# Kernel optimization log

Hardware: AMD Instinct MI355X
Metric: run time of the kernel (lower is better)

The kernel has to match this reference:

```python
import jax, jax.numpy as jnp
import numpy as np

# EventPropLinear constants (match init_kwargs)
DT = 1.0
TAU_M = 10.0
TAU_S = 1.0
AM = 1.0 - DT / TAU_M   # membrane decay
BM = DT / TAU_M         # membrane input coupling
AS = 1.0 - DT / TAU_S   # synaptic decay


def setup_inputs() -> dict:
    key = jax.random.key(0)
    k1, k2 = jax.random.split(key)
    T, B, IN, OUT = 128, 64, 1024, 1024
    x = jax.random.uniform(k1, (T, B, IN), dtype=jnp.float32)  # input drive / spikes in [0,1)
    # torch.nn.init.normal_(weight, mu, mu) with mu=0.1 -> mean 0.1, std 0.1
    weight = 0.1 + 0.1 * jax.random.normal(k2, (OUT, IN), dtype=jnp.float32)
    return {"x": x, "weight": weight}


def _forward_core(x, weight):
    # x: [T, B, IN]; weight: [OUT, IN]
    T, B, _ = x.shape
    O = weight.shape[0]
    # step i (1..T-1) uses input[i-1]; precompute the linear drive once
    cur = jnp.einsum('tbi,oi->tbo', x[:-1], weight)  # [T-1, B, OUT]

    def step(carry, c):
        V, I = carry
        Vn = AM * V + BM * I
        In = AS * I + c
        s = (Vn > 1.0).astype(x.dtype)
        Vn = (1.0 - s) * Vn           # reset on spike
        return (Vn, In), (s, In)

    z = jnp.zeros((B, O), x.dtype)
    _, (spk, Iseq) = jax.lax.scan(step, (z, z), cur)
    zrow = jnp.zeros((1, B, O), x.dtype)
    out = jnp.concatenate([zrow, spk], axis=0)      # output[0] = 0
    I_full = jnp.concatenate([zrow, Iseq], axis=0)  # I[0] = 0
    return out, I_full


def reference(x, weight):
    # returns spike train [T, B, OUT], matching torch output permuted back to time-major
    return _forward_core(x, weight)[0]
```

## Files before the change

kernel.cpp:

```cpp
#include <hip/hip_runtime.h>
#include <hip/hip_fp8.h>

typedef __attribute__((ext_vector_type(8))) short short8;
typedef __attribute__((ext_vector_type(4))) float f32x4;

__device__ __forceinline__ unsigned short f2bf(float f) {
    unsigned u = __float_as_uint(f);
    u += 0x7FFFu + ((u >> 16) & 1u);
    return (unsigned short)(u >> 16);
}

__device__ __forceinline__ unsigned char f2fp8(float f) {
    __hip_fp8_e4m3 q(f);
    return q.__x;
}

__global__ void eventprop_cvt8_kernel(const float* __restrict__ x, const float* __restrict__ w,
                                      unsigned char* __restrict__ x8, unsigned char* __restrict__ w8,
                                      const int nx, const int ntot)
{
    const int i = blockIdx.x * blockDim.x + threadIdx.x;
    const int e0 = i * 8;
    if (e0 >= ntot) return;
    const float* src;
    unsigned char* dst;
    if (e0 < nx) { src = x + e0; dst = x8 + e0; }
    else         { src = w + (e0 - nx); dst = w8 + (e0 - nx); }
    const float4 f0 = *(const float4*)(src);
    const float4 f1 = *(const float4*)(src + 4);
    uchar4 a, b;
    a.x = f2fp8(f0.x); a.y = f2fp8(f0.y); a.z = f2fp8(f0.z); a.w = f2fp8(f0.w);
    b.x = f2fp8(f1.x); b.y = f2fp8(f1.y); b.z = f2fp8(f1.z); b.w = f2fp8(f1.w);
    uint2 v;
    v.x = *(unsigned int*)&a;
    v.y = *(unsigned int*)&b;
    *(uint2*)dst = v;
}

__global__ __launch_bounds__(256, 4) void eventprop_gemm_scan_fp8_kernel(
    const unsigned char* __restrict__ X8, const unsigned char* __restrict__ W8,
    float* __restrict__ out, const int K, const int N, const int nbn)
{
    __shared__ __align__(16) unsigned char smem[33280];
    unsigned char* As = smem;
    unsigned char* Bs = smem + 16384;
    unsigned short* cur16 = (unsigned short*)smem;

    const int bid0 = blockIdx.x;
    const int cpx = gridDim.x >> 3;
    const int bid = (bid0 & 7) * cpx + (bid0 >> 3);
    const int bm = bid / nbn, bn = bid % nbn;
    const int n0 = bn * 128;

    const int tid = threadIdx.x;
    const int lane = tid & 63;
    const int wave = tid >> 6;
    const int wr = wave >> 1, wc = wave & 1;
    const int lrow = lane & 15, kg = lane >> 4;
    const int srow = lane >> 3;
    const int scol = (((lane & 7) ^ srow) * 16);

    f32x4 acc[4][4] = {};

    for (int kt = 0; kt < K; kt += 128) {
        #pragma unroll
        for (int jj = 0; jj < 4; ++jj) {
            const int j = wave * 4 + jj;
            const int trow = j * 8 + srow;
            const unsigned char* ga = &X8[(size_t)(trow * 64 + bm) * K + kt + scol];
            __builtin_amdgcn_global_load_lds(
                (const __attribute__((address_space(1))) unsigned int*)ga,
                (__attribute__((address_space(3))) unsigned int*)&As[j * 1024], 16, 0, 0);
        }
        #pragma unroll
        for (int jj = 0; jj < 4; ++jj) {
            const int j = wave * 4 + jj;
            const int row = j * 8 + srow;
            const unsigned char* gb = &W8[(size_t)(n0 + row) * K + kt + scol];
            __builtin_amdgcn_global_load_lds(
                (const __attribute__((address_space(1))) unsigned int*)gb,
                (__attribute__((address_space(3))) unsigned int*)&Bs[j * 1024], 16, 0, 0);
        }
        __syncthreads();

        const int rx = (lrow & 7) << 4;
        #pragma unroll
        for (int ks = 0; ks < 4; ++ks) {
            const int cc = (ks * 32 + kg * 8) ^ rx;
            long a[4], b[4];
            #pragma unroll
            for (int mi = 0; mi < 4; ++mi)
                a[mi] = *(const long*)&As[(wr * 64 + mi * 16 + lrow) * 128 + cc];
            #pragma unroll
            for (int ni = 0; ni < 4; ++ni)
                b[ni] = *(const long*)&Bs[(wc * 64 + ni * 16 + lrow) * 128 + cc];
            #pragma unroll
            for (int mi = 0; mi < 4; ++mi)
                #pragma unroll
                for (int ni = 0; ni < 4; ++ni)
                    acc[mi][ni] = __builtin_amdgcn_mfma_f32_16x16x32_fp8_fp8(
                        a[mi], b[ni], acc[mi][ni], 0, 0, 0);
        }
        __syncthreads();
    }

    const int r0 = kg * 4;
    #pragma unroll
    for (int mi = 0; mi < 4; ++mi) {
        #pragma unroll
        for (int ni = 0; ni < 4; ++ni) {
            #pragma unroll
            for (int r = 0; r < 4; ++r) {
                const int t = wr * 64 + mi * 16 + r0 + r;
                const int col = wc * 64 + ni * 16 + lrow;
                cur16[t * 130 + col] = f2bf(acc[mi][ni][r]);
            }
        }
    }
    __syncthreads();

    if (tid < 128) {
        const int col = tid;
        const size_t obase = (size_t)bm * N + n0 + col;
        const int BO = 64 * N;
        float V = 0.f, I = 0.f;
        float c[8];
        #pragma unroll
        for (int p = 0; p < 8; ++p)
            c[p] = __uint_as_float((unsigned int)cur16[p * 130 + col] << 16);
        out[obase] = 0.f;
        #pragma unroll 1
        for (int i = 0; i < 120; i += 8) {
            #pragma unroll
            for (int p = 0; p < 8; ++p) {
                const int it = i + p;
                const float cn = __uint_as_float((unsigned int)cur16[(it + 8) * 130 + col] << 16);
                const float Vn = 0.9f * V + 0.1f * I;
                const float s = (Vn > 1.0f) ? 1.0f : 0.0f;
                I = c[p];
                V = (1.0f - s) * Vn;
                out[(size_t)(it + 1) * BO + obase] = s;
                c[p] = cn;
            }
        }
        #pragma unroll
        for (int p = 0; p < 7; ++p) {
            const int it = 120 + p;
            const float Vn = 0.9f * V + 0.1f * I;
            const float s = (Vn > 1.0f) ? 1.0f : 0.0f;
            I = c[p];
            V = (1.0f - s) * Vn;
            out[(size_t)(it + 1) * BO + obase] = s;
        }
    }
}

__global__ __launch_bounds__(256, 2) void eventprop_gemm_f32in_kernel(
    const float* __restrict__ X, const float* __restrict__ W, float* __restrict__ C,
    const int K, const int N, const int nbn)
{
    __shared__ unsigned short As[128][32];
    __shared__ unsigned short Bs[128][32];
    const int bid = blockIdx.x;
    const int bm = bid / nbn, bn = bid % nbn;
    const int m0 = bm * 128, n0 = bn * 128;
    const int tid = threadIdx.x;
    const int lane = tid & 63;
    const int wave = tid >> 6;
    const int wr = wave >> 1, wc = wave & 1;
    const int lrow = lane & 15, kg = lane >> 4;

    f32x4 acc[4][4] = {};
    for (int kt = 0; kt < K; kt += 32) {
        #pragma unroll
        for (int p = 0; p < 4; ++p) {
            const int idx = p * 256 + tid;
            const int row = idx >> 3;
            const int c4  = (idx & 7) * 4;
            const float4 fa = *(const float4*)&X[(size_t)(m0 + row) * K + kt + c4];
            ushort4 ua; ua.x = f2bf(fa.x); ua.y = f2bf(fa.y); ua.z = f2bf(fa.z); ua.w = f2bf(fa.w);
            *(ushort4*)&As[row][c4] = ua;
            const float4 fb = *(const float4*)&W[(size_t)(n0 + row) * K + kt + c4];
            ushort4 ub; ub.x = f2bf(fb.x); ub.y = f2bf(fb.y); ub.z = f2bf(fb.z); ub.w = f2bf(fb.w);
            *(ushort4*)&Bs[row][c4] = ub;
        }
        __syncthreads();
        short8 a[4], b[4];
        #pragma unroll
        for (int mi = 0; mi < 4; ++mi) a[mi] = *(const short8*)&As[wr * 64 + mi * 16 + lrow][kg * 8];
        #pragma unroll
        for (int ni = 0; ni < 4; ++ni) b[ni] = *(const short8*)&Bs[wc * 64 + ni * 16 + lrow][kg * 8];
        #pragma unroll
        for (int mi = 0; mi < 4; ++mi)
            #pragma unroll
            for (int ni = 0; ni < 4; ++ni)
                acc[mi][ni] = __builtin_amdgcn_mfma_f32_16x16x32_bf16(a[mi], b[ni], acc[mi][ni], 0, 0, 0);
        __syncthreads();
    }
    const int r0 = kg * 4;
    #pragma unroll
    for (int mi = 0; mi < 4; ++mi)
        #pragma unroll
        for (int ni = 0; ni < 4; ++ni)
            #pragma unroll
            for (int r = 0; r < 4; ++r)
                C[(size_t)(m0 + wr * 64 + mi * 16 + r0 + r) * N + (n0 + wc * 64 + ni * 16 + lrow)] = acc[mi][ni][r];
}

__global__ void eventprop_scan_kernel(float* __restrict__ out, const int BO)
{
    const int idx = blockIdx.x * blockDim.x + threadIdx.x;
    float V = 0.f, I = 0.f;
    float c[8];
    #pragma unroll
    for (int p = 0; p < 8; ++p)
        c[p] = out[(size_t)p * BO + idx];
    out[idx] = 0.f;
    #pragma unroll 1
    for (int i = 0; i < 120; i += 8) {
        #pragma unroll
        for (int p = 0; p < 8; ++p) {
            const int it = i + p;
            const float cn = out[(size_t)(it + 8) * BO + idx];
            const float Vn = 0.9f * V + 0.1f * I;
            const float s = (Vn > 1.0f) ? 1.0f : 0.0f;
            I = c[p];
            V = (1.0f - s) * Vn;
            out[(size_t)(it + 1) * BO + idx] = s;
            c[p] = cn;
        }
    }
    #pragma unroll
    for (int p = 0; p < 7; ++p) {
        const int it = 120 + p;
        const float Vn = 0.9f * V + 0.1f * I;
        const float s = (Vn > 1.0f) ? 1.0f : 0.0f;
        I = c[p];
        V = (1.0f - s) * Vn;
        out[(size_t)(it + 1) * BO + idx] = s;
    }
}

extern "C" void kernel_launch(void* const* d_in, const int* in_sizes, int n_in,
                              void* d_out, int out_size, void* d_ws, size_t ws_size,
                              hipStream_t stream) {
    const float* x = (const float*)d_in[0];
    const float* w = (const float*)d_in[1];
    float* out = (float*)d_out;

    const int T = 128, B = 64, IN = 1024, OUT = 1024;
    const int Mpad = T * B;
    const int BO = B * OUT;
    const size_t nx = (size_t)Mpad * IN;
    const size_t nw = (size_t)OUT * IN;
    const size_t need = nx + nw;

    if (ws_size >= need) {
        unsigned char* x8 = (unsigned char*)d_ws;
        unsigned char* w8 = x8 + nx;
        const int ntot = (int)(nx + nw);
        const int cvt_blocks = (ntot / 8 + 255) / 256;
        eventprop_cvt8_kernel<<<dim3(cvt_blocks), dim3(256), 0, stream>>>(x, w, x8, w8, (int)nx, ntot);
        const int nbn = OUT / 128;
        const int nblocks = B * nbn;
        eventprop_gemm_scan_fp8_kernel<<<dim3(nblocks), dim3(256), 0, stream>>>(x8, w8, out, IN, OUT, nbn);
    } else {
        const int nbn = OUT / 128;
        const int nblocks = (Mpad / 128) * nbn;
        eventprop_gemm_f32in_kernel<<<dim3(nblocks), dim3(256), 0, stream>>>(x, w, out, IN, OUT, nbn);
        eventprop_scan_kernel<<<dim3(BO / 256), dim3(256), 0, stream>>>(out, BO);
    }
}
```

Before: 35.13 us.

## Shrink fused GEMM-scan N tile to 32 columns for more blocks

Reduces each block's output-column tile from 128 to 32, so the grid grows from 512 to 2048 blocks and the serial scan tail is spread across more blocks, with occupancy raised to 8 blocks per CU. Each wave now computes a 64x16 slab with one B fragment, and the staged currents are kept as fp32 in LDS instead of bf16. The trade-off is that the fp8 X tile is reloaded four times as often (lower reuse per MFMA), and only 32 threads per block run the scan.

Result: slower. 40.66 us (+15.7%).

```diff
diff --git a/kernel.cpp b/kernel.cpp
--- a/kernel.cpp
+++ b/kernel.cpp
@@ -37,20 +37,20 @@
     *(uint2*)dst = v;
 }
 
-__global__ __launch_bounds__(256, 4) void eventprop_gemm_scan_fp8_kernel(
+__global__ __launch_bounds__(256, 8) void eventprop_gemm_scan_fp8_kernel(
     const unsigned char* __restrict__ X8, const unsigned char* __restrict__ W8,
     float* __restrict__ out, const int K, const int N, const int nbn)
 {
-    __shared__ __align__(16) unsigned char smem[33280];
+    __shared__ __align__(16) unsigned char smem[20480];
     unsigned char* As = smem;
     unsigned char* Bs = smem + 16384;
-    unsigned short* cur16 = (unsigned short*)smem;
+    float* curLds = (float*)smem;
 
     const int bid0 = blockIdx.x;
     const int cpx = gridDim.x >> 3;
     const int bid = (bid0 & 7) * cpx + (bid0 >> 3);
     const int bm = bid / nbn, bn = bid % nbn;
-    const int n0 = bn * 128;
+    const int n0 = bn * 32;
 
     const int tid = threadIdx.x;
     const int lane = tid & 63;
@@ -60,7 +60,7 @@
     const int srow = lane >> 3;
     const int scol = (((lane & 7) ^ srow) * 16);
 
-    f32x4 acc[4][4] = {};
+    f32x4 acc[4] = {};
 
     for (int kt = 0; kt < K; kt += 128) {
         #pragma unroll
@@ -72,9 +72,8 @@
                 (const __attribute__((address_space(1))) unsigned int*)ga,
                 (__attribute__((address_space(3))) unsigned int*)&As[j * 1024], 16, 0, 0);
         }
-        #pragma unroll
-        for (int jj = 0; jj < 4; ++jj) {
-            const int j = wave * 4 + jj;
+        {
+            const int j = wave;
             const int row = j * 8 + srow;
             const unsigned char* gb = &W8[(size_t)(n0 + row) * K + kt + scol];
             __builtin_amdgcn_global_load_lds(
@@ -87,19 +86,14 @@
         #pragma unroll
         for (int ks = 0; ks < 4; ++ks) {
             const int cc = (ks * 32 + kg * 8) ^ rx;
-            long a[4], b[4];
+            long a[4], b;
             #pragma unroll
             for (int mi = 0; mi < 4; ++mi)
                 a[mi] = *(const long*)&As[(wr * 64 + mi * 16 + lrow) * 128 + cc];
-            #pragma unroll
-            for (int ni = 0; ni < 4; ++ni)
-                b[ni] = *(const long*)&Bs[(wc * 64 + ni * 16 + lrow) * 128 + cc];
+            b = *(const long*)&Bs[(wc * 16 + lrow) * 128 + cc];
             #pragma unroll
             for (int mi = 0; mi < 4; ++mi)
-                #pragma unroll
-                for (int ni = 0; ni < 4; ++ni)
-                    acc[mi][ni] = __builtin_amdgcn_mfma_f32_16x16x32_fp8_fp8(
-                        a[mi], b[ni], acc[mi][ni], 0, 0, 0);
+                acc[mi] = __builtin_amdgcn_mfma_f32_16x16x32_fp8_fp8(a[mi], b, acc[mi], 0, 0, 0);
         }
         __syncthreads();
     }
@@ -108,18 +102,15 @@
     #pragma unroll
     for (int mi = 0; mi < 4; ++mi) {
         #pragma unroll
-        for (int ni = 0; ni < 4; ++ni) {
-            #pragma unroll
-            for (int r = 0; r < 4; ++r) {
-                const int t = wr * 64 + mi * 16 + r0 + r;
-                const int col = wc * 64 + ni * 16 + lrow;
-                cur16[t * 130 + col] = f2bf(acc[mi][ni][r]);
-            }
+        for (int r = 0; r < 4; ++r) {
+            const int t = wr * 64 + mi * 16 + r0 + r;
+            const int col = wc * 16 + lrow;
+            curLds[t * 33 + col] = acc[mi][r];
         }
     }
     __syncthreads();
 
-    if (tid < 128) {
+    if (tid < 32) {
         const int col = tid;
         const size_t obase = (size_t)bm * N + n0 + col;
         const int BO = 64 * N;
@@ -127,14 +118,14 @@
         float c[8];
         #pragma unroll
         for (int p = 0; p < 8; ++p)
-            c[p] = __uint_as_float((unsigned int)cur16[p * 130 + col] << 16);
+            c[p] = curLds[p * 33 + col];
         out[obase] = 0.f;
         #pragma unroll 1
         for (int i = 0; i < 120; i += 8) {
             #pragma unroll
             for (int p = 0; p < 8; ++p) {
                 const int it = i + p;
-                const float cn = __uint_as_float((unsigned int)cur16[(it + 8) * 130 + col] << 16);
+                const float cn = curLds[(it + 8) * 33 + col];
                 const float Vn = 0.9f * V + 0.1f * I;
                 const float s = (Vn > 1.0f) ? 1.0f : 0.0f;
                 I = c[p];
@@ -261,7 +252,7 @@
         const int ntot = (int)(nx + nw);
         const int cvt_blocks = (ntot / 8 + 255) / 256;
         eventprop_cvt8_kernel<<<dim3(cvt_blocks), dim3(256), 0, stream>>>(x, w, x8, w8, (int)nx, ntot);
-        const int nbn = OUT / 128;
+        const int nbn = OUT / 32;
         const int nblocks = B * nbn;
         eventprop_gemm_scan_fp8_kernel<<<dim3(nblocks), dim3(256), 0, stream>>>(x8, w8, out, IN, OUT, nbn);
     } else {
```
